# Performance work log

Measured on AMD Instinct MI355X. Metric: run time of the kernel, lower is better.

The kernel has to match this reference:

```python
import jax, jax.numpy as jnp
import numpy as np
from jax import lax

BBOX_XFORM_CLIP = float(np.log(1000.0 / 16.0))
PRE_NMS_TOP_K = 1000
SCORE_THRESH = 0.05
IOU_THRESH = 0.5
MAX_DET = 100


def _decode_boxes(encoded, anchors):
    # encoded [...,4] = [dy,dx,dh,dw] with weights [10,10,5,5]; anchors [...,4] = [y1,x1,y2,x2]
    dy = encoded[..., 0] / 10.0
    dx = encoded[..., 1] / 10.0
    dh = jnp.minimum(encoded[..., 2] / 5.0, BBOX_XFORM_CLIP)
    dw = jnp.minimum(encoded[..., 3] / 5.0, BBOX_XFORM_CLIP)
    ah = anchors[..., 2] - anchors[..., 0]
    aw = anchors[..., 3] - anchors[..., 1]
    ayc = anchors[..., 0] + 0.5 * ah
    axc = anchors[..., 1] + 0.5 * aw
    yc = dy * ah + ayc
    xc = dx * aw + axc
    h = jnp.exp(dh) * ah
    w = jnp.exp(dw) * aw
    return jnp.stack([yc - 0.5 * h, xc - 0.5 * w, yc + 0.5 * h, xc + 0.5 * w], axis=-1)


def _clip_boxes(boxes, image_shape):
    # boxes [B,N,4]; image_shape [B,2] = (height, width)
    h = image_shape[..., 0:1]
    w = image_shape[..., 1:2]
    maxlen = jnp.concatenate([h, w, h, w], axis=-1)[:, None, :]  # [B,1,4]
    return jnp.clip(boxes, 0.0, maxlen)


def _nms_keep(boxes):
    # Greedy sequential NMS on score-sorted boxes [k,4]; returns keep mask [k].
    k = boxes.shape[0]
    y1, x1, y2, x2 = boxes[:, 0], boxes[:, 1], boxes[:, 2], boxes[:, 3]
    area = (y2 - y1) * (x2 - x1)
    idxs = jnp.arange(k)

    def body(keep, i):
        iy1 = jnp.maximum(y1[i], y1)
        ix1 = jnp.maximum(x1[i], x1)
        iy2 = jnp.minimum(y2[i], y2)
        ix2 = jnp.minimum(x2[i], x2)
        inter = jnp.maximum(iy2 - iy1, 0.0) * jnp.maximum(ix2 - ix1, 0.0)
        union = area[i] + area - inter
        iou = inter / jnp.where(union > 0, union, 1.0)
        suppressed = jnp.any(keep & (idxs < i) & (iou > IOU_THRESH))
        return keep.at[i].set(~suppressed), None

    keep, _ = lax.scan(body, jnp.zeros((k,), jnp.bool_), idxs)
    return keep


def _nms_single(boxes, scores):
    # boxes [k,4], scores [k] sorted descending; mirrors sorted_non_max_suppression_padded output.
    keep = _nms_keep(lax.stop_gradient(boxes))
    valid = keep & jnp.any(boxes > 0, axis=-1)  # zeroed (filtered) boxes never count
    sel = jnp.where(valid, scores, -jnp.inf)
    top_s, top_i = lax.top_k(sel, MAX_DET)
    out_valid = top_s > -jnp.inf
    out_scores = jnp.where(out_valid, top_s, 0.0)
    out_boxes = boxes[top_i] * out_valid[:, None].astype(boxes.dtype)
    return out_scores, out_boxes


def setup_inputs() -> dict:
    key = jax.random.key(0)
    k1, k2, k3, k4 = jax.random.split(key, 4)
    B, K, C = 8, 8192, 91
    raw_boxes = jax.random.normal(k1, (B, K, C * 4), jnp.float32) * 0.5
    raw_scores = jax.random.normal(k2, (B, K, C), jnp.float32) * 2.0
    # valid anchors [y1,x1,y2,x2] inside a 1024x1024 image
    ctr = jax.random.uniform(k3, (B, K, 2), jnp.float32, 0.0, 1024.0)
    sz = jax.random.uniform(k4, (B, K, 2), jnp.float32, 16.0, 128.0)
    anchor_boxes = jnp.concatenate([ctr - 0.5 * sz, ctr + 0.5 * sz], axis=-1)
    image_shape = jnp.full((B, 2), 1024.0, jnp.float32)
    return {"raw_boxes": raw_boxes, "raw_scores": raw_scores,
            "anchor_boxes": anchor_boxes, "image_shape": image_shape}


def reference(raw_boxes, raw_scores, anchor_boxes, image_shape):
    B, K, C = raw_scores.shape
    Cc = C - 1  # background removed

    probs = jax.nn.softmax(raw_scores, axis=-1)[:, :, 1:]           # [B,K,Cc]
    boxes = raw_boxes.reshape(B, K, C, 4)[:, :, 1:, :]              # [B,K,Cc,4]
    anch = jnp.broadcast_to(anchor_boxes[:, :, None, :], boxes.shape)
    dec = _decode_boxes(boxes.reshape(B, K * Cc, 4), anch.reshape(B, K * Cc, 4))
    dec = _clip_boxes(dec, image_shape).reshape(B, K, Cc, 4)

    # per-class top-k pre-NMS candidates (_select_top_k_scores + gather)
    k = min(K, PRE_NMS_TOP_K)
    s_t = jnp.transpose(probs, (0, 2, 1))                           # [B,Cc,K]
    top_s, top_i = lax.top_k(s_t, k)                                # [B,Cc,k]
    b_t = jnp.transpose(dec, (0, 2, 1, 3))                          # [B,Cc,K,4]
    top_b = jnp.take_along_axis(b_t, top_i[..., None], axis=2)      # [B,Cc,k,4]

    # filter_boxes_by_scores: score -> -1, box -> 0 below threshold
    mask = top_s > SCORE_THRESH
    top_s = jnp.where(mask, top_s, -1.0)
    top_b = top_b * mask[..., None].astype(top_b.dtype)

    nms_s, nms_b = jax.vmap(jax.vmap(_nms_single))(top_b, top_s)    # [B,Cc,MAX_DET], [B,Cc,MAX_DET,4]
    classes = jnp.broadcast_to(jnp.arange(Cc, dtype=jnp.int32)[None, :, None], nms_s.shape)

    all_s = nms_s.reshape(B, Cc * MAX_DET)
    all_b = nms_b.reshape(B, Cc * MAX_DET, 4)
    all_c = classes.reshape(B, Cc * MAX_DET)

    fin_s, fin_i = lax.top_k(all_s, MAX_DET)
    fin_b = jnp.take_along_axis(all_b, fin_i[..., None], axis=1)
    fin_c = jnp.take_along_axis(all_c, fin_i, axis=1) + 1           # restore background offset
    num = jnp.sum((fin_s > -1.0).astype(jnp.int32), axis=1)
    return fin_b, fin_s, fin_c, num
```

## Files before the change

kernel.cpp:

```cpp
#include <hip/hip_runtime.h>
#include <stdint.h>

typedef unsigned long long ull;

#define K_ANCH   8192
#define NCLS     91
#define NCC      90
#define B_SZ     8
#define CAP      1024
#define PRE_NMS  1000
#define MAXDET   100
#define NWMAX    16
#define NBW      128
#define SCORE_TH 0.05f
#define IOU_TH   0.5f
#define BBOX_CLIP 4.1351665565490723f

__device__ __forceinline__ float wave_max64(float v) {
  #pragma unroll
  for (int off = 32; off > 0; off >>= 1) v = fmaxf(v, __shfl_xor(v, off, 64));
  return v;
}
__device__ __forceinline__ float wave_sum64(float v) {
  #pragma unroll
  for (int off = 32; off > 0; off >>= 1) v += __shfl_xor(v, off, 64);
  return v;
}

__device__ __forceinline__ float4 decode_clip(float4 e, float4 a, float imh, float imw) {
#pragma clang fp contract(off)
  float dy = e.x / 10.0f;
  float dx = e.y / 10.0f;
  float dh = fminf(e.z / 5.0f, BBOX_CLIP);
  float dw = fminf(e.w / 5.0f, BBOX_CLIP);
  float ah = a.z - a.x;
  float aw = a.w - a.y;
  float ayc = a.x + 0.5f * ah;
  float axc = a.y + 0.5f * aw;
  float yc = dy * ah + ayc;
  float xc = dx * aw + axc;
  float h = expf(dh) * ah;
  float w = expf(dw) * aw;
  float y1 = yc - 0.5f * h, x1 = xc - 0.5f * w;
  float y2 = yc + 0.5f * h, x2 = xc + 0.5f * w;
  y1 = fminf(fmaxf(y1, 0.0f), imh);
  x1 = fminf(fmaxf(x1, 0.0f), imw);
  y2 = fminf(fmaxf(y2, 0.0f), imh);
  x2 = fminf(fmaxf(x2, 0.0f), imw);
  return make_float4(y1, x1, y2, x2);
}

__device__ __forceinline__ bool iou_gt(float4 bi, float ai, float4 bj, float aj) {
#pragma clang fp contract(off)
  float iy1 = fmaxf(bi.x, bj.x);
  float ix1 = fmaxf(bi.y, bj.y);
  float iy2 = fminf(bi.z, bj.z);
  float ix2 = fminf(bi.w, bj.w);
  float inter = fmaxf(iy2 - iy1, 0.0f) * fmaxf(ix2 - ix1, 0.0f);
  float uni = ai + aj - inter;
  float iou = inter / (uni > 0.0f ? uni : 1.0f);
  return iou > IOU_TH;
}

__global__ __launch_bounds__(1024) void kT_softmax(
    const float* __restrict__ raw_scores, const float* __restrict__ raw_boxes,
    const float4* __restrict__ anchors, const float* __restrict__ image_shape,
    float2* __restrict__ stats, ull* __restrict__ bmask,
    float* __restrict__ pstage, float4* __restrict__ bstage, int pcap)
{
  __shared__ ull    rowbits[64][2];
  __shared__ float  sp[64][92];
  __shared__ float4 sanch[64];
  __shared__ int    wl[5760];
  __shared__ int    wl_n;
  int tid = threadIdx.x;
  int wv = tid >> 6, lane = tid & 63;
  int b = blockIdx.x >> 7;
  int k0 = (blockIdx.x & 127) << 6;
  if (tid == 0) wl_n = 0;
  if (tid < 64) sanch[tid] = anchors[(size_t)b * K_ANCH + k0 + tid];
  #pragma unroll
  for (int i = 0; i < 4; i++) {
    int rl = (wv << 2) + i;
    int row = b * K_ANCH + k0 + rl;
    const float* srow = raw_scores + (size_t)row * NCLS;
    float s0 = srow[lane];
    bool has1 = lane < (NCLS - 64);
    float s1 = has1 ? srow[64 + lane] : -INFINITY;
    float m = wave_max64(fmaxf(s0, s1));
    float e0 = expf(s0 - m);
    float e1 = has1 ? expf(s1 - m) : 0.0f;
    float denom = wave_sum64(e0 + e1);
    float p0 = e0 / denom;
    float p1 = e1 / denom;
    sp[rl][lane] = p0;
    if (has1) sp[rl][64 + lane] = p1;
    ull b0 = __ballot(lane >= 1 && p0 > SCORE_TH);
    ull b1 = __ballot(has1 && p1 > SCORE_TH);
    if (lane == 0) {
      stats[row] = make_float2(m, denom);
      rowbits[rl][0] = b0;
      rowbits[rl][1] = b1;
    }
  }
  __syncthreads();
  if (tid < NCC) {
    int c = tid + 1, w = c >> 6, bit = c & 63;
    ull out = 0;
    #pragma unroll
    for (int r = 0; r < 64; r++)
      out |= ((rowbits[r][w] >> bit) & 1ull) << r;
    bmask[(size_t)(b * NCC + tid) * NBW + (k0 >> 6)] = out;
    int cnt = __popcll(out);
    if (cnt > 0) {
      int basei = atomicAdd(&wl_n, cnt);
      ull m = out;
      int rank = 0;
      while (m) {
        int r = __ffsll(m) - 1;
        m &= m - 1;
        wl[basei + rank] = (c << 12) | (r << 6) | rank;
        rank++;
      }
    }
  }
  __syncthreads();
  int nwl = wl_n;
  if (pcap > 0) {
    float imh = image_shape[b * 2 + 0];
    float imw = image_shape[b * 2 + 1];
    for (int t = tid; t < nwl; t += 1024) {
      int e = wl[t];
      int c = e >> 12, r = (e >> 6) & 63, rank = e & 63;
      if (rank >= pcap) continue;
      size_t row = (size_t)b * K_ANCH + k0 + r;
      float4 enc = ((const float4*)raw_boxes)[row * NCLS + c];
      float4 box = decode_clip(enc, sanch[r], imh, imw);
      size_t pw = (size_t)(b * NCC + (c - 1)) * NBW + (k0 >> 6);
      pstage[pw * pcap + rank] = sp[r][c];
      bstage[pw * pcap + rank] = box;
    }
  }
}

__global__ __launch_bounds__(256) void kN_nms(
    const float* __restrict__ raw_boxes, const float* __restrict__ raw_scores,
    const float4* __restrict__ anchors, const float* __restrict__ image_shape,
    const float2* __restrict__ stats, const ull* __restrict__ bmask,
    const float* __restrict__ pstage, const float4* __restrict__ bstage, int pcap,
    float* __restrict__ all_s, float4* __restrict__ all_b)
{
  __shared__ float4 sbox[PRE_NMS];
  __shared__ float  sarea[PRE_NMS];
  __shared__ float  sscore[PRE_NMS];
  __shared__ ull    sbuf[1056];
  __shared__ ull    sbm[NBW];
  __shared__ ull    skw[NWMAX];
  __shared__ int    soff[NBW];
  __shared__ int    swtot[2];
  __shared__ int    s_n;
  __shared__ int    s_done;

  int bc  = blockIdx.x;
  int tid = threadIdx.x;
  int b = bc / NCC;
  int c = bc - b * NCC + 1;
  int outbase = bc * MAXDET;
  size_t rowb = (size_t)b * K_ANCH;

  for (int i = tid; i < MAXDET; i += 256) {
    all_s[outbase + i] = 0.0f;
    all_b[outbase + i] = make_float4(0.f, 0.f, 0.f, 0.f);
  }
  if (tid < NWMAX) skw[tid] = 0ull;

  ull w0 = 0;
  int cnt = 0;
  if (tid < NBW) {
    w0 = bmask[(size_t)bc * NBW + tid];
    sbm[tid] = w0;
    cnt = __popcll(w0);
  }
  int incl = cnt;
  if (tid < 128) {
    int lane = tid & 63;
    #pragma unroll
    for (int d = 1; d < 64; d <<= 1) {
      int o = __shfl_up(incl, d, 64);
      if (lane >= d) incl += o;
    }
    if (lane == 63) swtot[tid >> 6] = incl;
  }
  if (tid == 0) s_done = 0;
  __syncthreads();
  if (tid < 128) soff[tid] = incl - cnt + ((tid >= 64) ? swtot[0] : 0);
  if (tid == 0) s_n = swtot[0] + swtot[1];
  __syncthreads();
  int n_load = min(s_n, CAP);

  if (tid < NBW) {
    int slot = soff[tid];
    ull m = w0;
    int kb = tid << 6;
    int rank = 0;
    size_t pw = (size_t)bc * NBW + tid;
    while (m) {
      int bit = __ffsll(m) - 1;
      m &= m - 1;
      int k = kb + bit;
      float p;
      if (rank < pcap) {
        p = pstage[pw * (size_t)pcap + rank];
      } else {
        size_t row = rowb + k;
        float s = raw_scores[row * NCLS + c];
        float2 md = stats[row];
        p = expf(s - md.x) / md.y;
      }
      if (slot < CAP)
        sbuf[slot] = ((ull)__float_as_uint(p) << 32) | (uint32_t)(K_ANCH - 1 - k);
      slot++;
      rank++;
    }
  }
  int n2 = (n_load <= 512) ? 512 : 1024;
  for (int i = n_load + tid; i < n2; i += 256) sbuf[i] = 0ull;
  __syncthreads();

  if (n_load <= 512) {
    ull e0 = sbuf[tid], e1 = sbuf[tid + 256];
    for (int size = 2; size <= 512; size <<= 1) {
      if (size == 512 && e0 < e1) { ull t = e0; e0 = e1; e1 = t; }
      for (int s = ((size >> 1) > 128 ? 128 : (size >> 1)); s >= 64; s >>= 1) {
        __syncthreads();
        sbuf[tid] = e0; sbuf[tid + 256] = e1;
        __syncthreads();
        ull p0 = sbuf[tid ^ s];
        ull p1 = sbuf[(tid + 256) ^ s];
        bool t0 = (((tid & s) == 0) == ((tid & size) == 0));
        bool t1 = ((((tid + 256) & s) == 0) == (((tid + 256) & size) == 0));
        e0 = t0 ? (e0 > p0 ? e0 : p0) : (e0 < p0 ? e0 : p0);
        e1 = t1 ? (e1 > p1 ? e1 : p1) : (e1 < p1 ? e1 : p1);
      }
      int smax = ((size >> 1) < 32 ? (size >> 1) : 32);
      for (int s = smax; s >= 1; s >>= 1) {
        ull p0 = __shfl_xor(e0, s, 64);
        ull p1 = __shfl_xor(e1, s, 64);
        bool t0 = (((tid & s) == 0) == ((tid & size) == 0));
        bool t1 = ((((tid + 256) & s) == 0) == (((tid + 256) & size) == 0));
        e0 = t0 ? (e0 > p0 ? e0 : p0) : (e0 < p0 ? e0 : p0);
        e1 = t1 ? (e1 > p1 ? e1 : p1) : (e1 < p1 ? e1 : p1);
      }
    }
    __syncthreads();
    sbuf[tid] = e0;
    sbuf[tid + 256] = e1;
    __syncthreads();
  } else {
    for (int size = 2; size <= 1024; size <<= 1) {
      for (int stride = size >> 1; stride > 0; stride >>= 1) {
        for (int i = tid; i < 1024; i += 256) {
          int j = i ^ stride;
          if (j > i) {
            ull ki = sbuf[i], kj = sbuf[j];
            bool desc = ((i & size) == 0);
            if (desc ? (ki < kj) : (ki > kj)) { sbuf[i] = kj; sbuf[j] = ki; }
          }
        }
        __syncthreads();
      }
    }
  }

  int n_use = min(n_load, PRE_NMS);
  float imh = image_shape[b * 2 + 0];
  float imw = image_shape[b * 2 + 1];
  for (int i = tid; i < n_use; i += 256) {
    ull key = sbuf[i];
    int k = K_ANCH - 1 - (int)(key & 0xFFFFFFFFull);
    int w = k >> 6;
    int rank = __popcll(sbm[w] & ((1ull << (k & 63)) - 1ull));
    float4 box;
    if (rank < pcap) {
      box = bstage[((size_t)bc * NBW + w) * (size_t)pcap + rank];
    } else {
      size_t row = rowb + k;
      float4 e = ((const float4*)raw_boxes)[row * NCLS + c];
      box = decode_clip(e, anchors[row], imh, imw);
    }
    sbox[i] = box;
    sscore[i] = __uint_as_float((uint32_t)(key >> 32));
    {
#pragma clang fp contract(off)
      sarea[i] = (box.z - box.x) * (box.w - box.y);
    }
  }

  int nwords_use = (n_use + 63) >> 6;
  int written = 0;
  for (int t = 0; t < nwords_use; t++) {
    __syncthreads();
    if (s_done) break;
    int j0 = t << 6;
    int j1 = min(j0 + 64, n_use);
    int r_lim = j1;

    for (int r = tid; r < r_lim; r += 256) {
      bool need = (r >= j0) || ((skw[r >> 6] >> (r & 63)) & 1ull);
      ull mrow = 0;
      if (need) {
        float4 br = sbox[r];
        float  ar = sarea[r];
        int js = max(j0, r + 1);
        for (int j = js; j < j1; j++)
          if (iou_gt(br, ar, sbox[j], sarea[j])) mrow |= 1ull << (j - j0);
      }
      sbuf[r] = mrow;
    }
    __syncthreads();

    if (tid < 64) {
      int lane = tid;
      ull acc = 0;
      for (int r = lane; r < j0; r += 64)
        if ((skw[r >> 6] >> (r & 63)) & 1ull) acc |= sbuf[r];
      #pragma unroll
      for (int off = 32; off > 0; off >>= 1) acc |= __shfl_xor(acc, off, 64);
      ull supp = acc;
      ull mj = (j0 + lane < n_use) ? sbuf[j0 + lane] : 0ull;
      bool vj = false;
      float4 bl;
      if (j0 + lane < n_use) {
        bl = sbox[j0 + lane];
        vj = (bl.x > 0.f || bl.y > 0.f || bl.z > 0.f || bl.w > 0.f);
      }
      ull vball = __ballot(vj);
      ull keptw = 0;
      int nrows = j1 - j0;
      for (int j = 0; j < nrows; j++) {
        if (!((supp >> j) & 1ull)) {
          keptw |= 1ull << j;
          supp |= __shfl(mj, j, 64);
          if ((vball >> j) & 1ull) {
            if (lane == 0) {
              int i = j0 + j;
              all_s[outbase + written] = sscore[i];
              all_b[outbase + written] = sbox[i];
            }
            written++;
            if (written == MAXDET) {
              if (lane == 0) s_done = 1;
              break;
            }
          }
        }
      }
      if (lane == 0) skw[t] = keptw;
    }
  }
}

__global__ __launch_bounds__(256) void k3_final(
    const float* __restrict__ all_s, const float4* __restrict__ all_b,
    float* __restrict__ out)
{
  __shared__ float ss[NCC * MAXDET];
  int b = blockIdx.x;
  int tid = threadIdx.x;
  const float* S = all_s + (size_t)b * NCC * MAXDET;
  for (int i = tid; i < NCC * MAXDET; i += 256) ss[i] = S[i];
  __syncthreads();
  if (tid >= 64) return;
  int lane = tid;

  float* fin_b = out;
  float* fin_s = out + B_SZ * MAXDET * 4;
  float* fin_c = fin_s + B_SZ * MAXDET;
  float* numo  = fin_c + B_SZ * MAXDET;

  int c0 = lane;
  int c1 = lane + 64;
  int p0 = 0, p1 = 0;
  ull cur0 = ((ull)__float_as_uint(ss[c0 * MAXDET]) << 32) | (uint32_t)(16383 - c0 * MAXDET);
  ull nxt0 = ((ull)__float_as_uint(ss[c0 * MAXDET + 1]) << 32) | (uint32_t)(16383 - (c0 * MAXDET + 1));
  ull cur1 = 0ull, nxt1 = 0ull;
  if (c1 < NCC) {
    cur1 = ((ull)__float_as_uint(ss[c1 * MAXDET]) << 32) | (uint32_t)(16383 - c1 * MAXDET);
    nxt1 = ((ull)__float_as_uint(ss[c1 * MAXDET + 1]) << 32) | (uint32_t)(16383 - (c1 * MAXDET + 1));
  }
  int cnt = 0;

  for (int step = 0; step < MAXDET; step++) {
    ull my = (cur0 > cur1) ? cur0 : cur1;
    ull g = my;
    #pragma unroll
    for (int off = 32; off > 0; off >>= 1) {
      ull o = __shfl_xor(g, off, 64);
      g = (o > g) ? o : g;
    }
    if (cur0 != 0ull && g == cur0) {
      p0++;
      cur0 = nxt0;
      int f = c0 * MAXDET + p0 + 1;
      nxt0 = (p0 + 1 < MAXDET)
           ? (((ull)__float_as_uint(ss[f]) << 32) | (uint32_t)(16383 - f)) : 0ull;
    } else if (cur1 != 0ull && g == cur1) {
      p1++;
      cur1 = nxt1;
      int f = c1 * MAXDET + p1 + 1;
      nxt1 = (p1 + 1 < MAXDET)
           ? (((ull)__float_as_uint(ss[f]) << 32) | (uint32_t)(16383 - f)) : 0ull;
    }

    if (lane == 0) {
      int flat = 16383 - (int)(g & 0xFFFFFFFFull);
      int cc = flat / MAXDET;
      float sc = __uint_as_float((uint32_t)(g >> 32));
      fin_s[b * MAXDET + step] = sc;
      fin_c[b * MAXDET + step] = (float)(cc + 1);
      float4 bx = all_b[(size_t)b * NCC * MAXDET + flat];
      ((float4*)fin_b)[b * MAXDET + step] = bx;
      if (sc > -1.0f) cnt++;
    }
  }
  if (lane == 0) numo[b] = (float)cnt;
}

extern "C" void kernel_launch(void* const* d_in, const int* in_sizes, int n_in,
                              void* d_out, int out_size, void* d_ws, size_t ws_size,
                              hipStream_t stream) {
  const float*  raw_boxes   = (const float*)d_in[0];
  const float*  raw_scores  = (const float*)d_in[1];
  const float4* anchors     = (const float4*)d_in[2];
  const float*  image_shape = (const float*)d_in[3];

  char* p = (char*)d_ws;
  size_t used = 0;
  auto alloc = [&](size_t bytes) {
    char* r = p + used;
    used += (bytes + 255) & ~(size_t)255;
    return r;
  };
  float2* stats = (float2*)alloc((size_t)B_SZ * K_ANCH * sizeof(float2));
  ull*    bmask = (ull*)   alloc((size_t)B_SZ * NCC * NBW * sizeof(ull));
  float*  all_s = (float*) alloc((size_t)B_SZ * NCC * MAXDET * sizeof(float));
  float4* all_b = (float4*)alloc((size_t)B_SZ * NCC * MAXDET * sizeof(float4));

  size_t nw = (size_t)B_SZ * NCC * NBW;
  int pcap = 16;
  while (pcap > 0 && used + ((nw * pcap * 4 + 255) & ~(size_t)255)
                          + ((nw * pcap * 16 + 255) & ~(size_t)255) > ws_size)
    pcap >>= 1;
  float*  pstage = (float*) alloc(nw * (size_t)pcap * 4);
  float4* bstage = (float4*)alloc(nw * (size_t)pcap * 16);

  kT_softmax<<<B_SZ * 128, 1024, 0, stream>>>(raw_scores, raw_boxes, anchors, image_shape,
                                              stats, bmask, pstage, bstage, pcap);
  kN_nms<<<B_SZ * NCC, 256, 0, stream>>>(raw_boxes, raw_scores, anchors, image_shape,
                                         stats, bmask, pstage, bstage, pcap, all_s, all_b);
  k3_final<<<B_SZ, 256, 0, stream>>>(all_s, all_b, (float*)d_out);
}
```

Baseline: 277.5 us.

## Replace serial final top-k merge with two-stage parallel bitonic selection

The final cross-class top-100 selection was a single-wave, 100-step sequential merge per batch. It is replaced with two kernels. The first sorts groups of 10 classes (1000 keys) with a block-wide bitonic sort across 72 blocks and keeps the top 100 of each. The second sorts the 900 surviving keys per batch and writes the outputs in parallel. This removes the serial dependency chain but adds an extra kernel launch and a global round trip for the intermediate keys.

```diff
diff --git a/kernel.cpp b/kernel.cpp
--- a/kernel.cpp
+++ b/kernel.cpp
@@ -12,6 +12,7 @@
 #define MAXDET   100
 #define NWMAX    16
 #define NBW      128
+#define NGRP     9
 #define SCORE_TH 0.05f
 #define IOU_TH   0.5f
 #define BBOX_CLIP 4.1351665565490723f
@@ -60,6 +61,22 @@
   float uni = ai + aj - inter;
   float iou = inter / (uni > 0.0f ? uni : 1.0f);
   return iou > IOU_TH;
+}
+
+__device__ __forceinline__ void bitonic1024(ull* sk, int tid) {
+  for (int size = 2; size <= 1024; size <<= 1) {
+    for (int stride = size >> 1; stride > 0; stride >>= 1) {
+      for (int i = tid; i < 1024; i += 256) {
+        int j = i ^ stride;
+        if (j > i) {
+          ull ki = sk[i], kj = sk[j];
+          bool desc = ((i & size) == 0);
+          if (desc ? (ki < kj) : (ki > kj)) { sk[i] = kj; sk[j] = ki; }
+        }
+      }
+      __syncthreads();
+    }
+  }
 }
 
 __global__ __launch_bounds__(1024) void kT_softmax(
@@ -257,19 +274,7 @@
     sbuf[tid + 256] = e1;
     __syncthreads();
   } else {
-    for (int size = 2; size <= 1024; size <<= 1) {
-      for (int stride = size >> 1; stride > 0; stride >>= 1) {
-        for (int i = tid; i < 1024; i += 256) {
-          int j = i ^ stride;
-          if (j > i) {
-            ull ki = sbuf[i], kj = sbuf[j];
-            bool desc = ((i & size) == 0);
-            if (desc ? (ki < kj) : (ki > kj)) { sbuf[i] = kj; sbuf[j] = ki; }
-          }
-        }
-        __syncthreads();
-      }
-    }
+    bitonic1024(sbuf, tid);
   }
 
   int n_use = min(n_load, PRE_NMS);
@@ -360,70 +365,61 @@
   }
 }
 
-__global__ __launch_bounds__(256) void k3_final(
-    const float* __restrict__ all_s, const float4* __restrict__ all_b,
+__global__ __launch_bounds__(256) void kG_group(
+    const float* __restrict__ all_s, ull* __restrict__ gkeys)
+{
+  __shared__ ull sk[1024];
+  int b = blockIdx.x / NGRP;
+  int g = blockIdx.x - b * NGRP;
+  int tid = threadIdx.x;
+  int flat0 = g * (NCC / NGRP) * MAXDET;
+  const float* S = all_s + (size_t)b * NCC * MAXDET;
+  for (int i = tid; i < 1024; i += 256) {
+    if (i < 1000) {
+      int flat = flat0 + i;
+      sk[i] = ((ull)__float_as_uint(S[flat]) << 32) | (uint32_t)(16383 - flat);
+    } else sk[i] = 0ull;
+  }
+  __syncthreads();
+  bitonic1024(sk, tid);
+  if (tid < MAXDET) gkeys[(size_t)blockIdx.x * MAXDET + tid] = sk[tid];
+}
+
+__global__ __launch_bounds__(256) void kF_final(
+    const ull* __restrict__ gkeys, const float4* __restrict__ all_b,
     float* __restrict__ out)
 {
-  __shared__ float ss[NCC * MAXDET];
+  __shared__ ull sk[1024];
+  __shared__ int swsum[4];
   int b = blockIdx.x;
   int tid = threadIdx.x;
-  const float* S = all_s + (size_t)b * NCC * MAXDET;
-  for (int i = tid; i < NCC * MAXDET; i += 256) ss[i] = S[i];
-  __syncthreads();
-  if (tid >= 64) return;
-  int lane = tid;
+  const ull* G = gkeys + (size_t)b * NGRP * MAXDET;
+  for (int i = tid; i < 1024; i += 256)
+    sk[i] = (i < NGRP * MAXDET) ? G[i] : 0ull;
+  __syncthreads();
+  bitonic1024(sk, tid);
 
   float* fin_b = out;
   float* fin_s = out + B_SZ * MAXDET * 4;
   float* fin_c = fin_s + B_SZ * MAXDET;
   float* numo  = fin_c + B_SZ * MAXDET;
 
-  int c0 = lane;
-  int c1 = lane + 64;
-  int p0 = 0, p1 = 0;
-  ull cur0 = ((ull)__float_as_uint(ss[c0 * MAXDET]) << 32) | (uint32_t)(16383 - c0 * MAXDET);
-  ull nxt0 = ((ull)__float_as_uint(ss[c0 * MAXDET + 1]) << 32) | (uint32_t)(16383 - (c0 * MAXDET + 1));
-  ull cur1 = 0ull, nxt1 = 0ull;
-  if (c1 < NCC) {
-    cur1 = ((ull)__float_as_uint(ss[c1 * MAXDET]) << 32) | (uint32_t)(16383 - c1 * MAXDET);
-    nxt1 = ((ull)__float_as_uint(ss[c1 * MAXDET + 1]) << 32) | (uint32_t)(16383 - (c1 * MAXDET + 1));
-  }
-  int cnt = 0;
-
-  for (int step = 0; step < MAXDET; step++) {
-    ull my = (cur0 > cur1) ? cur0 : cur1;
-    ull g = my;
-    #pragma unroll
-    for (int off = 32; off > 0; off >>= 1) {
-      ull o = __shfl_xor(g, off, 64);
-      g = (o > g) ? o : g;
-    }
-    if (cur0 != 0ull && g == cur0) {
-      p0++;
-      cur0 = nxt0;
-      int f = c0 * MAXDET + p0 + 1;
-      nxt0 = (p0 + 1 < MAXDET)
-           ? (((ull)__float_as_uint(ss[f]) << 32) | (uint32_t)(16383 - f)) : 0ull;
-    } else if (cur1 != 0ull && g == cur1) {
-      p1++;
-      cur1 = nxt1;
-      int f = c1 * MAXDET + p1 + 1;
-      nxt1 = (p1 + 1 < MAXDET)
-           ? (((ull)__float_as_uint(ss[f]) << 32) | (uint32_t)(16383 - f)) : 0ull;
-    }
-
-    if (lane == 0) {
-      int flat = 16383 - (int)(g & 0xFFFFFFFFull);
-      int cc = flat / MAXDET;
-      float sc = __uint_as_float((uint32_t)(g >> 32));
-      fin_s[b * MAXDET + step] = sc;
-      fin_c[b * MAXDET + step] = (float)(cc + 1);
-      float4 bx = all_b[(size_t)b * NCC * MAXDET + flat];
-      ((float4*)fin_b)[b * MAXDET + step] = bx;
-      if (sc > -1.0f) cnt++;
-    }
-  }
-  if (lane == 0) numo[b] = (float)cnt;
+  int v = 0;
+  if (tid < MAXDET) {
+    ull key = sk[tid];
+    int flat = 16383 - (int)(key & 0xFFFFFFFFull);
+    float sc = __uint_as_float((uint32_t)(key >> 32));
+    int cc = flat / MAXDET;
+    fin_s[b * MAXDET + tid] = sc;
+    fin_c[b * MAXDET + tid] = (float)(cc + 1);
+    ((float4*)fin_b)[b * MAXDET + tid] = all_b[(size_t)b * NCC * MAXDET + flat];
+    v = (sc > -1.0f) ? 1 : 0;
+  }
+  #pragma unroll
+  for (int off = 32; off > 0; off >>= 1) v += __shfl_xor(v, off, 64);
+  if ((tid & 63) == 0) swsum[tid >> 6] = v;
+  __syncthreads();
+  if (tid == 0) numo[b] = (float)(swsum[0] + swsum[1] + swsum[2] + swsum[3]);
 }
 
 extern "C" void kernel_launch(void* const* d_in, const int* in_sizes, int n_in,
@@ -445,6 +441,7 @@
   ull*    bmask = (ull*)   alloc((size_t)B_SZ * NCC * NBW * sizeof(ull));
   float*  all_s = (float*) alloc((size_t)B_SZ * NCC * MAXDET * sizeof(float));
   float4* all_b = (float4*)alloc((size_t)B_SZ * NCC * MAXDET * sizeof(float4));
+  ull*    gkeys = (ull*)   alloc((size_t)B_SZ * NGRP * MAXDET * sizeof(ull));
 
   size_t nw = (size_t)B_SZ * NCC * NBW;
   int pcap = 16;
@@ -458,5 +455,6 @@
                                               stats, bmask, pstage, bstage, pcap);
   kN_nms<<<B_SZ * NCC, 256, 0, stream>>>(raw_boxes, raw_scores, anchors, image_shape,
                                          stats, bmask, pstage, bstage, pcap, all_s, all_b);
-  k3_final<<<B_SZ, 256, 0, stream>>>(all_s, all_b, (float*)d_out);
-}
+  kG_group<<<B_SZ * NGRP, 256, 0, stream>>>(all_s, gkeys);
+  kF_final<<<B_SZ, 256, 0, stream>>>(gkeys, all_b, (float*)d_out);
+}
```

After: 286.5 us. 1.03x slower.
